# Kernel tuning notes

Measured on AMD Instinct MI355X. Metric: run time of the kernel, lower is better.

Reference implementation:

```python
import jax, jax.numpy as jnp
import numpy as np

B, S, HID = 1, 2048, 2048
H, KV, D = 16, 4, 128  # head_dim = HID // H; GQA group size g = H // KV
THETA = 10000.0


def setup_inputs() -> dict:
    key = jax.random.key(0)
    ks = jax.random.split(key, 5)
    s = 0.02  # initializer_range
    return {
        "hidden_states": jax.random.normal(ks[0], (B, S, HID), jnp.float32),
        "wq": jax.random.normal(ks[1], (HID, H * D), jnp.float32) * s,
        "wk": jax.random.normal(ks[2], (HID, KV * D), jnp.float32) * s,
        "wv": jax.random.normal(ks[3], (HID, KV * D), jnp.float32) * s,
        "wo": jax.random.normal(ks[4], (H * D, HID), jnp.float32) * s,
        "attention_mask": jnp.ones((B, S), jnp.int32),
        "position_ids": jnp.broadcast_to(jnp.arange(S, dtype=jnp.int32), (B, S)),
    }


def _rope(x, position_ids):
    # x: [b, s, h, d]; rotate consecutive (even, odd) pairs by angle t * theta^{-2j/d}
    half = D // 2
    inv_freq = 1.0 / (THETA ** (jnp.arange(0, D, 2, dtype=jnp.float32) / D))  # [half]
    ang = position_ids[..., None].astype(jnp.float32) * inv_freq  # [b, s, half]
    cos = jnp.cos(ang)[:, :, None, :]  # [b, s, 1, half]
    sin = jnp.sin(ang)[:, :, None, :]
    xr = x.astype(jnp.float32).reshape(*x.shape[:-1], half, 2)
    x0, x1 = xr[..., 0], xr[..., 1]
    out = jnp.stack((x0 * cos - x1 * sin, x0 * sin + x1 * cos), axis=-1)
    return out.reshape(x.shape)


def reference(hidden_states, wq, wk, wv, wo, attention_mask, position_ids):
    b, s, _ = hidden_states.shape
    g = H // KV
    xq = (hidden_states @ wq).reshape(b, s, H, D)
    xk = (hidden_states @ wk).reshape(b, s, KV, D)
    xv = (hidden_states @ wv).reshape(b, s, KV, D)
    # GQA: each kv head repeated g consecutive times -> H heads (matches einops '(h g)')
    xk = jnp.repeat(xk, g, axis=2)
    xv = jnp.repeat(xv, g, axis=2)
    xq = _rope(xq, position_ids)
    xk = _rope(xk, position_ids)
    # causal + padding mask -> additive bias (0 or -inf), softmax in fp32
    causal = jnp.tril(jnp.ones((s, s), dtype=bool))[None, None]  # [1,1,q,k]
    mask = causal & (attention_mask[:, None, None, :] > 0)  # [b,1,q,k]
    scores = jnp.einsum('bqhd,bkhd->bhqk', xq.astype(jnp.float32), xk.astype(jnp.float32))
    scores = scores / jnp.sqrt(jnp.float32(D))
    scores = jnp.where(mask, scores, jnp.finfo(jnp.float32).min)
    attn_weights = jax.nn.softmax(scores, axis=-1)  # [b,h,q,k] fp32
    attn = jnp.einsum('bhqk,bkhd->bqhd', attn_weights, xv.astype(jnp.float32))
    return (attn.reshape(b, s, H * D).astype(hidden_states.dtype)) @ wo
```

## Files before the change

### kernel.cpp

```cpp
#include <hip/hip_runtime.h>
#include <hip/hip_bf16.h>

#define S_LEN 2048
#define HIDDIM 2048
#define NH 16
#define NKV 4
#define HD 128
#define KVROW 1024
#define QKVN 3072

typedef __attribute__((ext_vector_type(8))) short short8;
typedef __attribute__((ext_vector_type(8))) unsigned short ushort8;
typedef __attribute__((ext_vector_type(4))) unsigned short ushort4v;
typedef __attribute__((ext_vector_type(4))) float f32x4;

__device__ __forceinline__ unsigned short f2bf(float f) {
  union { float f; unsigned int u; } v; v.f = f;
  unsigned int r = (v.u + 0x7FFFu + ((v.u >> 16) & 1u)) >> 16;
  return (unsigned short)r;
}
__device__ __forceinline__ float bf2f(unsigned short h) {
  union { unsigned int u; float f; } v; v.u = ((unsigned int)h) << 16;
  return v.f;
}

__device__ __forceinline__ void gl2lds16(const unsigned short* src,
                                         unsigned short* dst) {
  __builtin_amdgcn_global_load_lds(
      (const __attribute__((address_space(1))) unsigned int*)src,
      (__attribute__((address_space(3))) unsigned int*)dst, 16, 0, 0);
}

__device__ __forceinline__ void tw_body(
    const float* __restrict__ W, unsigned short* __restrict__ Wt,
    int Nsrc, int Kdst, int n_off, int bx, int by, int tid,
    unsigned short (*Ts)[72]) {
  const int n0 = bx * 64, k0 = by * 64;
  const int c2 = (tid & 31) * 2, rb = tid >> 5;
#pragma unroll
  for (int p = 0; p < 8; ++p) {
    int r = rb + p * 8;
    float2 v = *(const float2*)&W[(size_t)(k0 + r) * Nsrc + n0 + c2];
    Ts[c2][r] = f2bf(v.x);
    Ts[c2 + 1][r] = f2bf(v.y);
  }
  __syncthreads();
  const int n = tid >> 2, kq = (tid & 3) * 16;
  ushort8 w0 = *(const ushort8*)&Ts[n][kq];
  ushort8 w1 = *(const ushort8*)&Ts[n][kq + 8];
  size_t base = (size_t)(n_off + n0 + n) * Kdst + k0 + kq;
  *(ushort8*)&Wt[base] = w0;
  *(ushort8*)&Wt[base + 8] = w1;
}

__global__ __launch_bounds__(256) void prep_kernel(
    const float* __restrict__ H, unsigned short* __restrict__ Hb,
    const float* __restrict__ wq, const float* __restrict__ wk,
    const float* __restrict__ wv, unsigned short* __restrict__ WT1,
    const float* __restrict__ wo, unsigned short* __restrict__ WoT) {
  __shared__ unsigned short Ts[64][72];
  const int b = (int)blockIdx.x, tid = threadIdx.x;
  if (b < 2048) {
    int i = (b * 256 + tid) * 8;
    float4 a = *(const float4*)(H + i), c = *(const float4*)(H + i + 4);
    ushort8 r;
    r[0] = f2bf(a.x); r[1] = f2bf(a.y); r[2] = f2bf(a.z); r[3] = f2bf(a.w);
    r[4] = f2bf(c.x); r[5] = f2bf(c.y); r[6] = f2bf(c.z); r[7] = f2bf(c.w);
    *(ushort8*)(Hb + i) = r;
  } else if (b < 3072) {
    int t = b - 2048;
    tw_body(wq, WT1, HIDDIM, HIDDIM, 0, t & 31, t >> 5, tid, Ts);
  } else if (b < 3328) {
    int t = b - 3072;
    tw_body(wk, WT1, 512, HIDDIM, 2048, t & 7, t >> 3, tid, Ts);
  } else if (b < 3584) {
    int t = b - 3328;
    tw_body(wv, WT1, 512, HIDDIM, 2560, t & 7, t >> 3, tid, Ts);
  } else {
    int t = b - 3584;
    tw_body(wo, WoT, HIDDIM, HIDDIM, 0, t & 31, t >> 5, tid, Ts);
  }
}

__global__ __launch_bounds__(256) void transpose_w(
    const float* __restrict__ W, unsigned short* __restrict__ Wt,
    int Nsrc, int Kdst, int n_off) {
  __shared__ unsigned short Ts[64][72];
  tw_body(W, Wt, Nsrc, Kdst, n_off, (int)blockIdx.x, (int)blockIdx.y,
          (int)threadIdx.x, Ts);
}

__global__ __launch_bounds__(256) void tvrope_kernel(
    unsigned short* __restrict__ Qb, unsigned short* __restrict__ KVb,
    unsigned short* __restrict__ Vt, const int* __restrict__ pos,
    const int* __restrict__ amask, unsigned* __restrict__ mb) {
  __shared__ unsigned short Ts[64][72];
  const int b = (int)blockIdx.x, tid = threadIdx.x;
  if (b < 256) {
    const int c0 = (b & 7) * 64, s0 = (b >> 3) * 64;
    const int sr = tid >> 2, cq = (tid & 3) * 16;
    ushort8 a = *(const ushort8*)&KVb[(size_t)(s0 + sr) * KVROW + 512 + c0 + cq];
    ushort8 c = *(const ushort8*)&KVb[(size_t)(s0 + sr) * KVROW + 512 + c0 + cq + 8];
#pragma unroll
    for (int j = 0; j < 8; ++j) { Ts[cq + j][sr] = a[j]; Ts[cq + 8 + j][sr] = c[j]; }
    __syncthreads();
    const int cc = tid >> 2, sq = (tid & 3) * 16;
    ushort8 w0 = *(const ushort8*)&Ts[cc][sq];
    ushort8 w1 = *(const ushort8*)&Ts[cc][sq + 8];
    *(ushort8*)&Vt[(size_t)(c0 + cc) * S_LEN + s0 + sq] = w0;
    *(ushort8*)&Vt[(size_t)(c0 + cc) * S_LEN + s0 + sq + 8] = w1;
  } else if (b < 768) {
    int idx = (b - 256) * 256 + tid;
    int s = idx >> 6, j = idx & 63;
    float inv = exp2f(-0.2076205059304703f * (float)j);
    float ang = (float)pos[s] * inv;
    float sn, cs;
    __sincosf(ang, &sn, &cs);
    auto rot = [&](unsigned short* base) {
      unsigned* p = (unsigned*)base;
      unsigned v = *p;
      float x0 = bf2f((unsigned short)(v & 0xffff));
      float x1 = bf2f((unsigned short)(v >> 16));
      unsigned r = (unsigned)f2bf(x0 * cs - x1 * sn) |
                   ((unsigned)f2bf(x0 * sn + x1 * cs) << 16);
      *p = r;
    };
#pragma unroll
    for (int hh = 0; hh < NH; ++hh) rot(Qb + (size_t)s * HIDDIM + hh * HD + 2 * j);
#pragma unroll
    for (int hh = 0; hh < NKV; ++hh) rot(KVb + (size_t)s * KVROW + hh * HD + 2 * j);
  } else {
    if (tid < 64) {
      unsigned m = 0;
#pragma unroll
      for (int i = 0; i < 32; ++i) m |= (amask[tid * 32 + i] != 0 ? 1u : 0u) << i;
      mb[tid] = m;
    }
  }
}

template <bool CF>
__global__ __launch_bounds__(256) void gemm_tn(
    const unsigned short* __restrict__ A, const unsigned short* __restrict__ Bt,
    void* __restrict__ C1, void* __restrict__ C2,
    int M, int N, int K, int splitcol, int ld1, int ld2) {
  __shared__ unsigned short As[2][128 * 64];
  __shared__ unsigned short Bs[2][64 * 64];
  const int m0 = blockIdx.y * 128, n0 = blockIdx.x * 64;
  const int tid = threadIdx.x, wid = tid >> 6, lane = tid & 63;
  const int wr = wid >> 1, wc = wid & 1;
  const int lr = lane & 15, lg = lane >> 4;

  f32x4 acc[4][2];
#pragma unroll
  for (int m = 0; m < 4; ++m)
#pragma unroll
    for (int n = 0; n < 2; ++n) acc[m][n] = (f32x4){0.f, 0.f, 0.f, 0.f};

  const int srow = lane >> 3;
  const int scolb = (lane & 7) << 4;
  auto stage = [&](int k0, int b) {
#pragma unroll
    for (int j = 0; j < 4; ++j) {
      int row = wid * 32 + j * 8 + srow;
      int src = (scolb ^ ((row & 7) << 4)) >> 1;
      gl2lds16(A + (size_t)(m0 + row) * K + k0 + src,
               &As[b][(wid * 32 + j * 8) * 64]);
    }
#pragma unroll
    for (int j = 0; j < 2; ++j) {
      int row = wid * 16 + j * 8 + srow;
      int src = (scolb ^ ((row & 7) << 4)) >> 1;
      gl2lds16(Bt + (size_t)(n0 + row) * K + k0 + src,
               &Bs[b][(wid * 16 + j * 8) * 64]);
    }
  };

  stage(0, 0);
  int cur = 0;
  for (int k0 = 0; k0 < K; k0 += 64) {
    __syncthreads();
    if (k0 + 64 < K) stage(k0 + 64, cur ^ 1);
#pragma unroll
    for (int s = 0; s < 2; ++s) {
      short8 af[4], bfv[2];
#pragma unroll
      for (int m = 0; m < 4; ++m) {
        int row = wr * 64 + m * 16 + lr;
        int off = ((s * 64 + lg * 16) ^ ((row & 7) << 4)) >> 1;
        af[m] = *(const short8*)&As[cur][row * 64 + off];
      }
#pragma unroll
      for (int n = 0; n < 2; ++n) {
        int row = wc * 32 + n * 16 + lr;
        int off = ((s * 64 + lg * 16) ^ ((row & 7) << 4)) >> 1;
        bfv[n] = *(const short8*)&Bs[cur][row * 64 + off];
      }
#pragma unroll
      for (int m = 0; m < 4; ++m)
#pragma unroll
        for (int n = 0; n < 2; ++n)
          acc[m][n] = __builtin_amdgcn_mfma_f32_16x16x32_bf16(af[m], bfv[n], acc[m][n], 0, 0, 0);
    }
    cur ^= 1;
  }

#pragma unroll
  for (int m = 0; m < 4; ++m)
#pragma unroll
    for (int n = 0; n < 2; ++n)
#pragma unroll
      for (int r = 0; r < 4; ++r) {
        int row = m0 + wr * 64 + m * 16 + lg * 4 + r;
        int col = n0 + wc * 32 + n * 16 + lr;
        float v = acc[m][n][r];
        if (CF) ((float*)C1)[(size_t)row * ld1 + col] = v;
        else if (col < splitcol) ((unsigned short*)C1)[(size_t)row * ld1 + col] = f2bf(v);
        else ((unsigned short*)C2)[(size_t)row * ld2 + (col - splitcol)] = f2bf(v);
      }
}

__global__ __launch_bounds__(256) void attn_kernel(
    const unsigned short* __restrict__ Qb, const unsigned short* __restrict__ KVb,
    const unsigned short* __restrict__ VtG, const unsigned* __restrict__ mbits,
    unsigned short* __restrict__ Ob,
    unsigned short* __restrict__ Opart, float* __restrict__ Lpart, int nsplit) {
  const int d = (int)blockIdx.x;
  const int kvh = (d & 7) >> 1;
  const int x = ((d >> 3) << 1) | (d & 1);
  const int qt = 63 - (x >> 2);
  const int c = x & 3;
  const int nch = (qt >> 4) + 1;
  if (nsplit == 0) { if (c != 0) return; }
  else if (c >= nch) return;
  const int qb = qt * 32;
  int kbeg = 0, kend = qb + 32;
  bool partial = false;
  if (nsplit && nch > 1) {
    kbeg = c * 512;
    kend = min(kend, kbeg + 512);
    partial = true;
  }

  __shared__ unsigned short Klds[2][32 * 128];
  __shared__ unsigned short Vlds[2][128 * 32];
  __shared__ unsigned short Plds[4][32][40];
  const int tid = threadIdx.x, wid = tid >> 6, lane = tid & 63;
  const int lr = lane & 15, lg = lane >> 4;
  const int h = kvh * 4 + wid;

  short8 qfa[4], qfb[4];
  {
    const unsigned short* qpa = Qb + (size_t)(qb + lr) * HIDDIM + h * HD;
    const unsigned short* qpb = Qb + (size_t)(qb + 16 + lr) * HIDDIM + h * HD;
#pragma unroll
    for (int cc = 0; cc < 4; ++cc) {
      qfa[cc] = *(const short8*)(qpa + cc * 32 + lg * 8);
      qfb[cc] = *(const short8*)(qpb + cc * 32 + lg * 8);
    }
  }
  f32x4 oa[8], ob[8];
#pragma unroll
  for (int cc = 0; cc < 8; ++cc) {
    oa[cc] = (f32x4){0.f, 0.f, 0.f, 0.f};
    ob[cc] = (f32x4){0.f, 0.f, 0.f, 0.f};
  }
  float lsa = 0.f, lsb = 0.f;

  const unsigned short* Vg = VtG + (size_t)(kvh * HD) * S_LEN;

  const int ksr_ = lane >> 4;
  const int kscb = (lane & 15) << 4;
  const int vsr_ = lane >> 2;
  const int vscb = (lane & 3) << 4;

  auto stage = [&](int kt, int b) {
#pragma unroll
    for (int j = 0; j < 2; ++j) {
      int krow = wid * 8 + j * 4 + ksr_;
      int ksrc = (kscb ^ ((krow & 7) << 4)) >> 1;
      gl2lds16(KVb + (size_t)(kt + krow) * KVROW + kvh * HD + ksrc,
               &Klds[b][(wid * 8 + j * 4) * 128]);
      int vrow = wid * 32 + j * 16 + vsr_;
      int vsrc = (vscb ^ ((vrow & 3) << 4)) >> 1;
      gl2lds16(Vg + (size_t)vrow * S_LEN + kt + vsrc,
               &Vlds[b][(wid * 32 + j * 16) * 32]);
    }
  };

  stage(kbeg, 0);

  const int qra = qb + lr, qrb = qb + 16 + lr;
  const float SCALE = 0.08838834764831845f;
  int cur = 0;

  for (int kt = kbeg; kt < kend; kt += 32) {
    __syncthreads();
    if (kt + 32 < kend) stage(kt + 32, cur ^ 1);

    f32x4 sa[2], sb[2];
#pragma unroll
    for (int t = 0; t < 2; ++t) {
      sa[t] = (f32x4){0.f, 0.f, 0.f, 0.f};
      sb[t] = (f32x4){0.f, 0.f, 0.f, 0.f};
    }
    const unsigned short* kbase = &Klds[cur][0];
    __builtin_amdgcn_s_setprio(1);
#pragma unroll
    for (int t = 0; t < 2; ++t)
#pragma unroll
      for (int cc = 0; cc < 4; ++cc) {
        short8 kf = *(const short8*)(kbase + ((t * 16 + lr) << 7) +
                                     ((((cc << 6) + (lg << 4)) ^ ((lr & 7) << 4)) >> 1));
        sa[t] = __builtin_amdgcn_mfma_f32_16x16x32_bf16(kf, qfa[cc], sa[t], 0, 0, 0);
        sb[t] = __builtin_amdgcn_mfma_f32_16x16x32_bf16(kf, qfb[cc], sb[t], 0, 0, 0);
      }
    __builtin_amdgcn_s_setprio(0);
    const unsigned mw = mbits[kt >> 5];
    float pa[2][4], pb[2][4];
    if ((kt + 31 <= qb) && (mw == ~0u)) {
#pragma unroll
      for (int t = 0; t < 2; ++t)
#pragma unroll
        for (int r = 0; r < 4; ++r) {
          float va = __expf(sa[t][r] * SCALE - 3.0f);
          float vb = __expf(sb[t][r] * SCALE - 3.0f);
          pa[t][r] = va; lsa += va;
          pb[t][r] = vb; lsb += vb;
        }
    } else {
#pragma unroll
      for (int t = 0; t < 2; ++t)
#pragma unroll
        for (int r = 0; r < 4; ++r) {
          int kk = t * 16 + lg * 4 + r;
          bool okm = (mw >> kk) & 1u;
          float va = __expf((okm && kt + kk <= qra) ? sa[t][r] * SCALE - 3.0f : -1e30f);
          float vb = __expf((okm && kt + kk <= qrb) ? sb[t][r] * SCALE - 3.0f : -1e30f);
          pa[t][r] = va; lsa += va;
          pb[t][r] = vb; lsb += vb;
        }
    }
#pragma unroll
    for (int t = 0; t < 2; ++t) {
      ushort4v pka, pkb;
#pragma unroll
      for (int r = 0; r < 4; ++r) { pka[r] = f2bf(pa[t][r]); pkb[r] = f2bf(pb[t][r]); }
      *(ushort4v*)&Plds[wid][lr][t * 16 + lg * 4] = pka;
      *(ushort4v*)&Plds[wid][16 + lr][t * 16 + lg * 4] = pkb;
    }
    short8 pfa = *(const short8*)&Plds[wid][lr][lg * 8];
    short8 pfb = *(const short8*)&Plds[wid][16 + lr][lg * 8];
    const unsigned short* vbase = &Vlds[cur][0];
    __builtin_amdgcn_s_setprio(1);
#pragma unroll
    for (int cc = 0; cc < 8; ++cc) {
      short8 vf = *(const short8*)(vbase + ((cc * 16 + lr) << 5) +
                                   ((lg ^ (lr & 3)) << 3));
      oa[cc] = __builtin_amdgcn_mfma_f32_16x16x32_bf16(pfa, vf, oa[cc], 0, 0, 0);
      ob[cc] = __builtin_amdgcn_mfma_f32_16x16x32_bf16(pfb, vf, ob[cc], 0, 0, 0);
    }
    __builtin_amdgcn_s_setprio(0);
    cur ^= 1;
  }

  float la = lsa;
  la += __shfl_xor(la, 16, 64);
  la += __shfl_xor(la, 32, 64);
  float lb = lsb;
  lb += __shfl_xor(lb, 16, 64);
  lb += __shfl_xor(lb, 32, 64);

  if (!partial) {
    float lra[4], lrb[4];
#pragma unroll
    for (int r = 0; r < 4; ++r) {
      lra[r] = 1.0f / __shfl(la, lg * 4 + r, 16);
      lrb[r] = 1.0f / __shfl(lb, lg * 4 + r, 16);
    }
#pragma unroll
    for (int cc = 0; cc < 8; ++cc)
#pragma unroll
      for (int r = 0; r < 4; ++r) {
        const int rowa = qb + lg * 4 + r;
        const int rowb = qb + 16 + lg * 4 + r;
        Ob[(size_t)rowa * HIDDIM + h * HD + cc * 16 + lr] = f2bf(oa[cc][r] * lra[r]);
        Ob[(size_t)rowb * HIDDIM + h * HD + cc * 16 + lr] = f2bf(ob[cc][r] * lrb[r]);
      }
  } else {
    const int g = qt >> 4, j = qt & 15;
    const int base = (g == 1) ? 0 : (g == 2) ? 32 : 80;
    const int slot = base + j * nch + c + 144 * kvh;
    if (lg == 0) {
      Lpart[slot * 128 + wid * 32 + lr] = la;
      Lpart[slot * 128 + wid * 32 + 16 + lr] = lb;
    }
#pragma unroll
    for (int cc = 0; cc < 8; ++cc)
#pragma unroll
      for (int r = 0; r < 4; ++r) {
        Opart[(size_t)slot * 16384 + wid * 4096 +
              (lg * 4 + r) * 128 + cc * 16 + lr] = f2bf(oa[cc][r]);
        Opart[(size_t)slot * 16384 + wid * 4096 +
              (16 + lg * 4 + r) * 128 + cc * 16 + lr] = f2bf(ob[cc][r]);
      }
  }
}

__global__ __launch_bounds__(256) void combine_kernel(
    const unsigned short* __restrict__ Opart, const float* __restrict__ Lpart,
    unsigned short* __restrict__ Ab) {
  const int qt = 16 + (int)blockIdx.x;
  const int kvh = (int)blockIdx.y;
  const int nch = (qt >> 4) + 1;
  const int g = qt >> 4, j = qt & 15;
  const int base = (g == 1) ? 0 : (g == 2) ? 32 : 80;
  const int s0 = base + j * nch + 144 * kvh;
  const int tid = threadIdx.x;
  const int rowid = tid >> 1;
  const int d0 = (tid & 1) * 64;
  float L = 0.f;
  for (int cc = 0; cc < nch; ++cc) L += Lpart[(s0 + cc) * 128 + rowid];
  const float linv = 1.0f / L;
  const int h = kvh * 4 + (rowid >> 5);
  const int row = qt * 32 + (rowid & 31);
  unsigned short* dst = Ab + (size_t)row * HIDDIM + h * HD + d0;
  for (int i = 0; i < 64; i += 8) {
    float acc[8] = {0, 0, 0, 0, 0, 0, 0, 0};
    for (int cc = 0; cc < nch; ++cc) {
      ushort8 v = *(const ushort8*)&Opart[(size_t)(s0 + cc) * 16384 +
                                          rowid * 128 + d0 + i];
#pragma unroll
      for (int k = 0; k < 8; ++k) acc[k] += bf2f(v[k]);
    }
    ushort8 r;
#pragma unroll
    for (int k = 0; k < 8; ++k) r[k] = f2bf(acc[k] * linv);
    *(ushort8*)(dst + i) = r;
  }
}

extern "C" void kernel_launch(void* const* d_in, const int* in_sizes, int n_in,
                              void* d_out, int out_size, void* d_ws, size_t ws_size,
                              hipStream_t stream) {
  const float* hidden = (const float*)d_in[0];
  const float* wq = (const float*)d_in[1];
  const float* wk = (const float*)d_in[2];
  const float* wv = (const float*)d_in[3];
  const float* wo = (const float*)d_in[4];
  const int* amask = (const int*)d_in[5];
  const int* pos = (const int*)d_in[6];

  unsigned short* Qb = (unsigned short*)d_ws;
  unsigned short* KVb = Qb + (size_t)S_LEN * HIDDIM;
  unsigned short* Ab = KVb + (size_t)S_LEN * KVROW;
  unsigned short* WT1 = Ab + (size_t)S_LEN * HIDDIM;
  unsigned short* Hb = WT1 + (size_t)QKVN * HIDDIM;
  float* out = (float*)d_out;

  unsigned short* Opart = WT1;
  unsigned short* Vt_chunk = WT1 + (size_t)576 * 16384;
  unsigned* mbits_chunk = (unsigned*)((char*)d_ws + 41943040ull);
  float* Lpart = (float*)((char*)d_ws + 41943296ull);
  const size_t need_chunk = 42238208ull;
  unsigned short* WoT2 = (unsigned short*)((char*)d_ws + 42238208ull);
  const size_t need_tier2 = 42238208ull + 8388608ull;
  unsigned short* Vt_fb = WT1 + (size_t)HIDDIM * HIDDIM;
  unsigned* mbits_fb = (unsigned*)((char*)d_ws + 31457280ull);

  const int nsplit = (ws_size >= need_chunk) ? 1 : 0;
  const int tier2 = (ws_size >= need_tier2) ? 1 : 0;
  unsigned short* Vt = nsplit ? Vt_chunk : Vt_fb;
  unsigned* mbits = nsplit ? mbits_chunk : mbits_fb;
  unsigned short* WoT = tier2 ? WoT2 : WT1;

  dim3 blk(256);
  prep_kernel<<<tier2 ? 4608 : 3584, blk, 0, stream>>>(
      hidden, Hb, wq, wk, wv, WT1, wo, WoT2);
  gemm_tn<false><<<dim3(QKVN / 64, S_LEN / 128), blk, 0, stream>>>(
      Hb, WT1, Qb, KVb, S_LEN, QKVN, HIDDIM, 2048, HIDDIM, KVROW);
  tvrope_kernel<<<769, blk, 0, stream>>>(Qb, KVb, Vt, pos, amask, mbits);
  attn_kernel<<<dim3(1024), blk, 0, stream>>>(
      Qb, KVb, Vt, mbits, Ab, Opart, Lpart, nsplit);
  if (nsplit)
    combine_kernel<<<dim3(48, NKV), blk, 0, stream>>>(Opart, Lpart, Ab);
  if (!tier2)
    transpose_w<<<dim3(32, 32), blk, 0, stream>>>(wo, WT1, HIDDIM, HIDDIM, 0);
  gemm_tn<true><<<dim3(HIDDIM / 64, S_LEN / 128), blk, 0, stream>>>(
      Ab, WoT, out, nullptr, S_LEN, HIDDIM, HIDDIM, HIDDIM, HIDDIM, 0);
}
```

Before: 152.8 us.

## Fuse RoPE and V transpose into QKV GEMM epilogue, fold mask bits into prep

Adds a specialized QKV GEMM whose epilogue applies rotary embedding to Q and K in registers, using a lane shuffle to pair even and odd columns, and writes V directly in transposed layout. The attention-mask bit packing moves into an extra block of the prep kernel. Together these remove the separate tvrope kernel launch and its extra read/write pass over Q, K and V. This path is used only when the workspace is large enough. The epilogue adds sincos work per element and strided transposed stores.

```diff
diff --git a/kernel.cpp b/kernel.cpp
--- a/kernel.cpp
+++ b/kernel.cpp
@@ -57,7 +57,8 @@
     const float* __restrict__ H, unsigned short* __restrict__ Hb,
     const float* __restrict__ wq, const float* __restrict__ wk,
     const float* __restrict__ wv, unsigned short* __restrict__ WT1,
-    const float* __restrict__ wo, unsigned short* __restrict__ WoT) {
+    const float* __restrict__ wo, unsigned short* __restrict__ WoT,
+    const int* __restrict__ amask, unsigned* __restrict__ mb) {
   __shared__ unsigned short Ts[64][72];
   const int b = (int)blockIdx.x, tid = threadIdx.x;
   if (b < 2048) {
@@ -76,9 +77,16 @@
   } else if (b < 3584) {
     int t = b - 3328;
     tw_body(wv, WT1, 512, HIDDIM, 2560, t & 7, t >> 3, tid, Ts);
-  } else {
+  } else if (b < 4608) {
     int t = b - 3584;
     tw_body(wo, WoT, HIDDIM, HIDDIM, 0, t & 31, t >> 5, tid, Ts);
+  } else {
+    if (tid < 64) {
+      unsigned m = 0;
+#pragma unroll
+      for (int i = 0; i < 32; ++i) m |= (amask[tid * 32 + i] != 0 ? 1u : 0u) << i;
+      mb[tid] = m;
+    }
   }
 }
 
@@ -220,6 +228,111 @@
       }
 }
 
+__global__ __launch_bounds__(256) void gemm_qkv(
+    const unsigned short* __restrict__ A, const unsigned short* __restrict__ Bt,
+    unsigned short* __restrict__ Qb, unsigned short* __restrict__ KVb,
+    unsigned short* __restrict__ Vt, const int* __restrict__ pos) {
+  __shared__ unsigned short As[2][128 * 64];
+  __shared__ unsigned short Bs[2][64 * 64];
+  const int K = HIDDIM;
+  const int m0 = blockIdx.y * 128, n0 = blockIdx.x * 64;
+  const int tid = threadIdx.x, wid = tid >> 6, lane = tid & 63;
+  const int wr = wid >> 1, wc = wid & 1;
+  const int lr = lane & 15, lg = lane >> 4;
+
+  f32x4 acc[4][2];
+#pragma unroll
+  for (int m = 0; m < 4; ++m)
+#pragma unroll
+    for (int n = 0; n < 2; ++n) acc[m][n] = (f32x4){0.f, 0.f, 0.f, 0.f};
+
+  const int srow = lane >> 3;
+  const int scolb = (lane & 7) << 4;
+  auto stage = [&](int k0, int b) {
+#pragma unroll
+    for (int j = 0; j < 4; ++j) {
+      int row = wid * 32 + j * 8 + srow;
+      int src = (scolb ^ ((row & 7) << 4)) >> 1;
+      gl2lds16(A + (size_t)(m0 + row) * K + k0 + src,
+               &As[b][(wid * 32 + j * 8) * 64]);
+    }
+#pragma unroll
+    for (int j = 0; j < 2; ++j) {
+      int row = wid * 16 + j * 8 + srow;
+      int src = (scolb ^ ((row & 7) << 4)) >> 1;
+      gl2lds16(Bt + (size_t)(n0 + row) * K + k0 + src,
+               &Bs[b][(wid * 16 + j * 8) * 64]);
+    }
+  };
+
+  stage(0, 0);
+  int cur = 0;
+  for (int k0 = 0; k0 < K; k0 += 64) {
+    __syncthreads();
+    if (k0 + 64 < K) stage(k0 + 64, cur ^ 1);
+#pragma unroll
+    for (int s = 0; s < 2; ++s) {
+      short8 af[4], bfv[2];
+#pragma unroll
+      for (int m = 0; m < 4; ++m) {
+        int row = wr * 64 + m * 16 + lr;
+        int off = ((s * 64 + lg * 16) ^ ((row & 7) << 4)) >> 1;
+        af[m] = *(const short8*)&As[cur][row * 64 + off];
+      }
+#pragma unroll
+      for (int n = 0; n < 2; ++n) {
+        int row = wc * 32 + n * 16 + lr;
+        int off = ((s * 64 + lg * 16) ^ ((row & 7) << 4)) >> 1;
+        bfv[n] = *(const short8*)&Bs[cur][row * 64 + off];
+      }
+#pragma unroll
+      for (int m = 0; m < 4; ++m)
+#pragma unroll
+        for (int n = 0; n < 2; ++n)
+          acc[m][n] = __builtin_amdgcn_mfma_f32_16x16x32_bf16(af[m], bfv[n], acc[m][n], 0, 0, 0);
+    }
+    cur ^= 1;
+  }
+
+  if (n0 < 2560) {
+    const bool isQ = (n0 < 2048);
+    const bool odd = lr & 1;
+#pragma unroll
+    for (int n = 0; n < 2; ++n) {
+      const int col = n0 + wc * 32 + n * 16 + lr;
+      const int j = (col & 127) >> 1;
+      const float inv = exp2f(-0.2076205059304703f * (float)j);
+#pragma unroll
+      for (int m = 0; m < 4; ++m)
+#pragma unroll
+        for (int r = 0; r < 4; ++r) {
+          const int row = m0 + wr * 64 + m * 16 + lg * 4 + r;
+          float own = acc[m][n][r];
+          float other = __shfl_xor(own, 1, 64);
+          float ang = (float)pos[row] * inv;
+          float sn, cs;
+          __sincosf(ang, &sn, &cs);
+          float out = odd ? (other * sn + own * cs) : (own * cs - other * sn);
+          if (isQ) Qb[(size_t)row * HIDDIM + col] = f2bf(out);
+          else KVb[(size_t)row * KVROW + (col - 2048)] = f2bf(out);
+        }
+    }
+  } else {
+#pragma unroll
+    for (int n = 0; n < 2; ++n) {
+      const int vcol = n0 + wc * 32 + n * 16 + lr - 2560;
+#pragma unroll
+      for (int m = 0; m < 4; ++m) {
+        const int row0 = m0 + wr * 64 + m * 16 + lg * 4;
+        ushort4v pk;
+#pragma unroll
+        for (int r = 0; r < 4; ++r) pk[r] = f2bf(acc[m][n][r]);
+        *(ushort4v*)&Vt[(size_t)vcol * S_LEN + row0] = pk;
+      }
+    }
+  }
+}
+
 __global__ __launch_bounds__(256) void attn_kernel(
     const unsigned short* __restrict__ Qb, const unsigned short* __restrict__ KVb,
     const unsigned short* __restrict__ VtG, const unsigned* __restrict__ mbits,
@@ -465,21 +578,30 @@
   const size_t need_chunk = 42238208ull;
   unsigned short* WoT2 = (unsigned short*)((char*)d_ws + 42238208ull);
   const size_t need_tier2 = 42238208ull + 8388608ull;
+  unsigned short* Vt3 = (unsigned short*)((char*)d_ws + 50626816ull);
+  const size_t need_tier3 = 50626816ull + 2097152ull;
   unsigned short* Vt_fb = WT1 + (size_t)HIDDIM * HIDDIM;
   unsigned* mbits_fb = (unsigned*)((char*)d_ws + 31457280ull);
 
   const int nsplit = (ws_size >= need_chunk) ? 1 : 0;
   const int tier2 = (ws_size >= need_tier2) ? 1 : 0;
-  unsigned short* Vt = nsplit ? Vt_chunk : Vt_fb;
+  const int tier3 = (ws_size >= need_tier3) ? 1 : 0;
+  unsigned short* Vt = tier3 ? Vt3 : (nsplit ? Vt_chunk : Vt_fb);
   unsigned* mbits = nsplit ? mbits_chunk : mbits_fb;
   unsigned short* WoT = tier2 ? WoT2 : WT1;
 
   dim3 blk(256);
-  prep_kernel<<<tier2 ? 4608 : 3584, blk, 0, stream>>>(
-      hidden, Hb, wq, wk, wv, WT1, wo, WoT2);
-  gemm_tn<false><<<dim3(QKVN / 64, S_LEN / 128), blk, 0, stream>>>(
-      Hb, WT1, Qb, KVb, S_LEN, QKVN, HIDDIM, 2048, HIDDIM, KVROW);
-  tvrope_kernel<<<769, blk, 0, stream>>>(Qb, KVb, Vt, pos, amask, mbits);
+  int prep_blocks = tier3 ? 4609 : (tier2 ? 4608 : 3584);
+  prep_kernel<<<prep_blocks, blk, 0, stream>>>(
+      hidden, Hb, wq, wk, wv, WT1, wo, WoT2, amask, mbits);
+  if (tier3) {
+    gemm_qkv<<<dim3(QKVN / 64, S_LEN / 128), blk, 0, stream>>>(
+        Hb, WT1, Qb, KVb, Vt, pos);
+  } else {
+    gemm_tn<false><<<dim3(QKVN / 64, S_LEN / 128), blk, 0, stream>>>(
+        Hb, WT1, Qb, KVb, S_LEN, QKVN, HIDDIM, 2048, HIDDIM, KVROW);
+    tvrope_kernel<<<769, blk, 0, stream>>>(Qb, KVb, Vt, pos, amask, mbits);
+  }
   attn_kernel<<<dim3(1024), blk, 0, stream>>>(
       Qb, KVb, Vt, mbits, Ab, Opart, Lpart, nsplit);
   if (nsplit)
```

Result: no change. 154.6 us (+1.2%).
